# Performance work log

Measured on AMD Instinct MI355X. Metric: run time of the kernel, lower is better.

Reference implementation:

```python
import jax, jax.numpy as jnp
import numpy as np
import math

ALPHA, BETA = 0.0, 0.1  # MarketRelation defaults


def setup_inputs() -> dict:
    key = jax.random.key(0)
    ks = jax.random.split(key, 15)
    n, T, d, K, C = 1024, 8, 64, 8, 64
    h = d  # hidden = (2*infeat)//2 = infeat
    s = 0.1
    u = jax.random.uniform(ks[13], (n, n, K), jnp.float32, 1e-6, 1.0 - 1e-6)
    return {
        "x":   jax.random.normal(ks[0], (n, T, d), jnp.float32),
        "Ind": jax.random.uniform(ks[1], (n, n), jnp.float32),
        "Loc": jax.random.uniform(ks[2], (n, n), jnp.float32),
        "a":   jax.random.normal(ks[3], (T, 1), jnp.float32),
        "W1m": jax.random.normal(ks[4], (2 * d, h), jnp.float32) * s,
        "b1m": jax.random.normal(ks[5], (h,), jnp.float32) * s,
        "W2m": jax.random.normal(ks[6], (h, 1), jnp.float32) * s,
        "b2m": jax.random.normal(ks[7], (1,), jnp.float32) * s,
        "W1s": jax.random.normal(ks[8], (2 * d, h), jnp.float32) * s,
        "b1s": jax.random.normal(ks[9], (h,), jnp.float32) * s,
        "W2s": jax.random.normal(ks[10], (h, K), jnp.float32) * s,
        "b2s": jax.random.normal(ks[11], (K,), jnp.float32) * s,
        "E":   jax.random.normal(ks[12], (K, n, C), jnp.float32) * s,
        "g":   -jnp.log(-jnp.log(u)),  # Gumbel(0,1) noise for gumbel_softmax
    }


def reference(x, Ind, Loc, a, W1m, b1m, W2m, b2m, W1s, b1s, W2s, b2s, E, g):
    n, T, d = x.shape
    # --- MarketRelation ---
    # fc1(concat(x_j, x_k)) == x_j @ W1m[:d] + x_k @ W1m[d:] + b1m (same math,
    # avoids materializing the N x N x 2d concat tensor)
    W1a, W1b = W1m[:d], W1m[d:]
    a_soft = jax.nn.softmax(a, axis=0)  # [T,1]
    A_mkt = jnp.zeros((n, n), x.dtype)
    for i in range(T):
        xi = x[:, i, :]                      # [n,d]
        hA = xi @ W1a                        # [n,h]
        hB = xi @ W1b                        # [n,h]
        hmat = jax.nn.relu(hA[:, None, :] + hB[None, :, :] + b1m)  # [n,n,h]
        adj = jax.nn.relu(hmat @ W2m + b2m)[..., 0]                # [n,n]
        factor = 1.0 + ALPHA * math.exp(-BETA * (T - i - 1))
        A_mkt = A_mkt + adj * (a_soft[i, 0] * factor)
    # --- NobsRelation (on last timestep) ---
    xl = x[:, -1, :]
    Ws1a, Ws1b = W1s[:d], W1s[d:]
    hs = jax.nn.relu((xl @ Ws1a)[:, None, :] + (xl @ Ws1b)[None, :, :] + b1s)
    logits = jax.nn.relu(hs @ W2s + b2s)          # [n,n,K]
    y = jax.nn.softmax(logits + g, axis=-1)       # gumbel_softmax, tau=1, soft
    D = jnp.einsum('knc,kmc->nmk', E, E)          # stack of E_k E_k^T, [n,n,K]
    A_nobs = jnp.sum(D * y, axis=-1)              # [n,n]
    return jnp.stack([Ind, Loc, A_mkt, A_nobs])   # [4,n,n]
```

## Files before the change

kernel.cpp:

```cpp
#include <hip/hip_runtime.h>

typedef unsigned short USH;
typedef unsigned int UIN;
typedef _Float16 F16;
typedef F16 h2 __attribute__((ext_vector_type(2)));
typedef short bfrag __attribute__((ext_vector_type(8)));
typedef float f32x4 __attribute__((ext_vector_type(4)));

__device__ __forceinline__ float bf2f(USH u) {
    return __uint_as_float(((unsigned int)u) << 16);
}
__device__ __forceinline__ USH f2bf(float f) {
    unsigned int i = __float_as_uint(f);
    i += 0x7FFFu + ((i >> 16) & 1u);
    return (USH)(i >> 16);
}
__device__ __forceinline__ UIN pkh2(float a, float b) {
    h2 h; h.x = (F16)a; h.y = (F16)b;
    return __builtin_bit_cast(UIN, h);
}
__device__ __forceinline__ h2 u2h(UIN u) { return __builtin_bit_cast(h2, u); }
__device__ __forceinline__ h2 relu2h(h2 s) {
    const h2 zz = {(F16)0.0f, (F16)0.0f};
    return __builtin_elementwise_max(s, zz);
}
__device__ __forceinline__ float fdot2(h2 a, h2 b, float c) {
#if __has_builtin(__builtin_amdgcn_fdot2)
    return __builtin_amdgcn_fdot2(a, b, c, false);
#else
    return c + (float)a.x * (float)b.x + (float)a.y * (float)b.y;
#endif
}

__device__ __forceinline__ float ldf(const void* p, long idx, int bf) {
    return bf ? bf2f(((const USH*)p)[idx]) : ((const float*)p)[idx];
}
__device__ __forceinline__ void ld4(const void* p, long idx, int bf, float o[4]) {
    if (bf) {
        ushort4 u = *(const ushort4*)((const USH*)p + idx);
        o[0] = bf2f(u.x); o[1] = bf2f(u.y); o[2] = bf2f(u.z); o[3] = bf2f(u.w);
    } else {
        float4 v = *(const float4*)((const float*)p + idx);
        o[0] = v.x; o[1] = v.y; o[2] = v.z; o[3] = v.w;
    }
}

__device__ __forceinline__ int detect_bf(const void* ind) {
    const uint4* p = (const uint4*)ind;
    unsigned o = 0;
    #pragma unroll
    for (int i = 0; i < 8; ++i) { uint4 v = p[i]; o |= v.x | v.y | v.z | v.w; }
    return (o & 0x8000u) == 0;
}


__global__ __launch_bounds__(256) void k_pre_d(
    const void* __restrict__ x,
    const void* __restrict__ W1m,
    const void* __restrict__ b1m,
    const void* __restrict__ W1s,
    const void* __restrict__ b1s,
    const void* __restrict__ E,
    const void* __restrict__ IndDet,
    UIN* __restrict__ hA16,
    UIN* __restrict__ hB16,
    USH* __restrict__ D)
{
    __shared__ float smem[8192];
    const int bf = detect_bf(IndDet);
    const int tid = threadIdx.x;
    const int bid = blockIdx.x;

    if (bid < 512) {
        USH* sE = (USH*)smem;
        const int k = bid >> 6;
        const int nb = ((bid >> 3) & 7) * 128, mb = (bid & 7) * 128;
        const long ek = (long)k * 65536;

        const int row = tid >> 1;
        const int c0 = (tid & 1) * 32;
        #pragma unroll
        for (int side = 0; side < 2; ++side) {
            const int rbase = side ? mb : nb;
            USH* sDst = sE + side * 8192;
            const long gbase = ek + (long)(rbase + row) * 64 + c0;
            USH tmp[32];
            if (bf) {
                #pragma unroll
                for (int q = 0; q < 4; ++q)
                    *(uint4*)&tmp[q * 8] = *(const uint4*)((const USH*)E + gbase + q * 8);
            } else {
                #pragma unroll
                for (int q = 0; q < 4; ++q) {
                    const float4 va = *(const float4*)((const float*)E + gbase + q * 8);
                    const float4 vb = *(const float4*)((const float*)E + gbase + q * 8 + 4);
                    tmp[q * 8 + 0] = f2bf(va.x); tmp[q * 8 + 1] = f2bf(va.y);
                    tmp[q * 8 + 2] = f2bf(va.z); tmp[q * 8 + 3] = f2bf(va.w);
                    tmp[q * 8 + 4] = f2bf(vb.x); tmp[q * 8 + 5] = f2bf(vb.y);
                    tmp[q * 8 + 6] = f2bf(vb.z); tmp[q * 8 + 7] = f2bf(vb.w);
                }
            }
            #pragma unroll
            for (int q = 0; q < 4; ++q) {
                const int byte = (c0 + q * 8) * 2;
                const int sw = (row * 128 + (byte ^ ((row & 7) << 4))) >> 1;
                *(uint4*)&sDst[sw] = *(uint4*)&tmp[q * 8];
            }
        }
        __syncthreads();

        const int lane = tid & 63;
        const int w = tid >> 6;
        const int wn = (w >> 1) * 64, wm = (w & 1) * 64;
        const int fr = lane & 15, kg = lane >> 4;

        f32x4 acc[4][4] = {};
        #pragma unroll
        for (int ks = 0; ks < 2; ++ks) {
            const int cb = (ks * 32 + kg * 8) * 2;
            bfrag af[4], bfv[4];
            #pragma unroll
            for (int f = 0; f < 4; ++f) {
                const int ra = wn + f * 16 + fr;
                af[f] = *(const bfrag*)&sE[(ra * 128 + (cb ^ ((ra & 7) << 4))) >> 1];
                const int rb = wm + f * 16 + fr;
                bfv[f] = *(const bfrag*)&sE[8192 + ((rb * 128 + (cb ^ ((rb & 7) << 4))) >> 1)];
            }
            #pragma unroll
            for (int fn = 0; fn < 4; ++fn)
                #pragma unroll
                for (int fm = 0; fm < 4; ++fm)
                    acc[fn][fm] = __builtin_amdgcn_mfma_f32_16x16x32_bf16(
                        af[fn], bfv[fm], acc[fn][fm], 0, 0, 0);
        }

        USH* Dk = D + ((long)k << 20);
        #pragma unroll
        for (int fn = 0; fn < 4; ++fn) {
            const int nrow = nb + wn + fn * 16 + kg * 4;
            #pragma unroll
            for (int fm = 0; fm < 4; ++fm) {
                const int mcol = mb + wm + fm * 16 + fr;
                #pragma unroll
                for (int r = 0; r < 4; ++r)
                    Dk[(long)(nrow + r) * 1024 + mcol] = f2bf(acc[fn][fm][r]);
            }
        }
    } else {
        float* sA = smem;
        float* sB = smem + 4096;
        const int tx = tid & 15, ty = tid >> 4;
        const int bid2 = bid - 512;
        const int nbase = (bid2 & 15) * 64;
        const int by = bid2 >> 4;
        int t, rb;
        const void* Wsrc;
        const void* bias;
        UIN* dst;
        if (by < 8)        { t = by;     rb = 0;  Wsrc = W1m; bias = nullptr; dst = hA16 + by * 32768; }
        else if (by < 16)  { t = by - 8; rb = 64; Wsrc = W1m; bias = b1m;     dst = hB16 + (by - 8) * 32768; }
        else if (by == 16) { t = 7;      rb = 0;  Wsrc = W1s; bias = nullptr; dst = hA16 + 8 * 32768; }
        else               { t = 7;      rb = 64; Wsrc = W1s; bias = b1s;     dst = hB16 + 8 * 32768; }

        {
            const int n_l = tid >> 2, dq = tid & 3;
            const long base = (long)(nbase + n_l) * 512 + t * 64 + dq * 16;
            #pragma unroll
            for (int j = 0; j < 4; ++j) {
                float o[4]; ld4(x, base + j * 4, bf, o);
                const int d0 = dq * 16 + j * 4;
                #pragma unroll
                for (int e = 0; e < 4; ++e) sA[(d0 + e) * 64 + n_l] = o[e];
            }
        }
        {
            const int d_l = tid >> 2, cq = tid & 3;
            const long base = (long)(rb + d_l) * 64 + cq * 16;
            #pragma unroll
            for (int j = 0; j < 4; ++j) {
                float o[4]; ld4(Wsrc, base + j * 4, bf, o);
                const int c0 = cq * 16 + j * 4;
                #pragma unroll
                for (int e = 0; e < 4; ++e) sB[d_l * 64 + c0 + e] = o[e];
            }
        }
        __syncthreads();

        const int c0 = tx * 4, nq = ty * 4;
        float acc[4][4] = {};
        #pragma unroll 16
        for (int d = 0; d < 64; ++d) {
            const float4 xa = *(const float4*)&sA[d * 64 + nq];
            const float4 wv = *(const float4*)&sB[d * 64 + c0];
            const float aa[4] = {xa.x, xa.y, xa.z, xa.w};
            const float ww[4] = {wv.x, wv.y, wv.z, wv.w};
            #pragma unroll
            for (int ci = 0; ci < 4; ++ci)
                #pragma unroll
                for (int ni = 0; ni < 4; ++ni)
                    acc[ci][ni] += ww[ci] * aa[ni];
        }
        float b[4] = {0.f, 0.f, 0.f, 0.f};
        if (bias) {
            #pragma unroll
            for (int ci = 0; ci < 4; ++ci) b[ci] = ldf(bias, c0 + ci, bf);
        }
        const int cp0 = c0 >> 1;
        #pragma unroll
        for (int ni = 0; ni < 4; ++ni) {
            const int col = nbase + nq + ni;
            dst[cp0 * 1024 + col]       = pkh2(acc[0][ni] + b[0], acc[1][ni] + b[1]);
            dst[(cp0 + 1) * 1024 + col] = pkh2(acc[2][ni] + b[2], acc[3][ni] + b[3]);
        }
    }
}

__global__ __launch_bounds__(256, 4) void k_main(
    const UIN* __restrict__ hA16,
    const UIN* __restrict__ hB16,
    const USH* __restrict__ Dm,
    const void* __restrict__ Ind, const void* __restrict__ Loc,
    const void* __restrict__ a, const void* __restrict__ W2m,
    const void* __restrict__ b2m, const void* __restrict__ W2s,
    const void* __restrict__ b2s, const void* __restrict__ g,
    void* __restrict__ out)
{
    __shared__ UIN As[2][1024];
    __shared__ UIN Bs[2][1024];
    __shared__ UIN w2m16[32];
    __shared__ UIN w2s16[256];
    __shared__ float asoft_l[8];

    const int bf = detect_bf(Ind);
    const int tid = threadIdx.x;
    const int mb = blockIdx.x * 32, nb = blockIdx.y * 32;
    const int tx = tid & 15, ty = tid >> 4;
    const int m0 = tx * 2, n0 = ty * 2;

    if (tid < 32) w2m16[tid] = pkh2(ldf(W2m, 2 * tid, bf), ldf(W2m, 2 * tid + 1, bf));
    if (tid >= 64 && tid < 96) {
        const int cp = tid - 64;
        #pragma unroll
        for (int k = 0; k < 8; ++k)
            w2s16[cp * 8 + k] = pkh2(ldf(W2s, (2 * cp) * 8 + k, bf),
                                     ldf(W2s, (2 * cp + 1) * 8 + k, bf));
    }
    if (tid < 8) {
        float av[8], mx = -1e30f, s = 0.0f;
        #pragma unroll
        for (int k = 0; k < 8; ++k) { av[k] = ldf(a, k, bf); mx = fmaxf(mx, av[k]); }
        #pragma unroll
        for (int k = 0; k < 8; ++k) s += __expf(av[k] - mx);
        asoft_l[tid] = __expf(av[tid] - mx) / s;
    }
    const float b2m_f = ldf(b2m, 0, bf);

    const int offA = (tid >> 3) * 1024 + nb + (tid & 7) * 4;
    const int offB = (tid >> 3) * 1024 + mb + (tid & 7) * 4;
    const int ldsOff = (tid >> 3) * 32 + (tid & 7) * 4;

    {
        const uint4 pa = *(const uint4*)(hA16 + offA);
        const uint4 pb = *(const uint4*)(hB16 + offB);
        *(uint4*)&As[0][ldsOff] = pa;
        *(uint4*)&Bs[0][ldsOff] = pb;
    }
    __syncthreads();

    float amk[2][2] = {{0.f, 0.f}, {0.f, 0.f}};

    for (int t = 0; t < 8; ++t) {
        const int cur = t & 1, nxt = cur ^ 1;
        const uint4 pa = *(const uint4*)(hA16 + (t + 1) * 32768 + offA);
        const uint4 pb = *(const uint4*)(hB16 + (t + 1) * 32768 + offB);

        float a00 = 0.f, a01 = 0.f, a10 = 0.f, a11 = 0.f;
        #pragma unroll
        for (int cp = 0; cp < 32; ++cp) {
            const uint2 au = *(const uint2*)&As[cur][(cp << 5) + n0];
            const uint2 bu = *(const uint2*)&Bs[cur][(cp << 5) + m0];
            const h2 wv = u2h(w2m16[cp]);
            const h2 a0 = u2h(au.x), a1 = u2h(au.y);
            const h2 b0 = u2h(bu.x), b1 = u2h(bu.y);
            const h2 z00 = relu2h(a0 + b0), z01 = relu2h(a0 + b1);
            const h2 z10 = relu2h(a1 + b0), z11 = relu2h(a1 + b1);
            a00 = fdot2(z00, wv, a00); a01 = fdot2(z01, wv, a01);
            a10 = fdot2(z10, wv, a10); a11 = fdot2(z11, wv, a11);
        }
        const float as_t = asoft_l[t];
        amk[0][0] += fmaxf(a00 + b2m_f, 0.f) * as_t;
        amk[0][1] += fmaxf(a01 + b2m_f, 0.f) * as_t;
        amk[1][0] += fmaxf(a10 + b2m_f, 0.f) * as_t;
        amk[1][1] += fmaxf(a11 + b2m_f, 0.f) * as_t;

        *(uint4*)&As[nxt][ldsOff] = pa;
        *(uint4*)&Bs[nxt][ldsOff] = pb;
        __syncthreads();
    }

    float lg[2][2][8];
    #pragma unroll
    for (int i = 0; i < 2; ++i)
        #pragma unroll
        for (int j = 0; j < 2; ++j)
            #pragma unroll
            for (int k = 0; k < 8; ++k) lg[i][j][k] = 0.f;

    #pragma unroll 8
    for (int cp = 0; cp < 32; ++cp) {
        const uint2 au = *(const uint2*)&As[0][(cp << 5) + n0];
        const uint2 bu = *(const uint2*)&Bs[0][(cp << 5) + m0];
        const h2 a0 = u2h(au.x), a1 = u2h(au.y);
        const h2 b0 = u2h(bu.x), b1 = u2h(bu.y);
        const h2 z00 = relu2h(a0 + b0), z01 = relu2h(a0 + b1);
        const h2 z10 = relu2h(a1 + b0), z11 = relu2h(a1 + b1);
        const uint4 wa = *(const uint4*)&w2s16[cp * 8];
        const uint4 wb = *(const uint4*)&w2s16[cp * 8 + 4];
        const UIN wks[8] = {wa.x, wa.y, wa.z, wa.w, wb.x, wb.y, wb.z, wb.w};
        #pragma unroll
        for (int k = 0; k < 8; ++k) {
            const h2 wv = u2h(wks[k]);
            lg[0][0][k] = fdot2(z00, wv, lg[0][0][k]);
            lg[0][1][k] = fdot2(z01, wv, lg[0][1][k]);
            lg[1][0][k] = fdot2(z10, wv, lg[1][0][k]);
            lg[1][1][k] = fdot2(z11, wv, lg[1][1][k]);
        }
    }

    float b2s_f[8];
    #pragma unroll
    for (int k = 0; k < 8; ++k) b2s_f[k] = ldf(b2s, k, bf);

    #pragma unroll
    for (int i = 0; i < 2; ++i) {
        const long rowoff = (long)(nb + n0 + i) * 1024 + mb + m0;
        float gv[16];
        ld4(g, rowoff * 8 + 0, bf, gv + 0);
        ld4(g, rowoff * 8 + 4, bf, gv + 4);
        ld4(g, rowoff * 8 + 8, bf, gv + 8);
        ld4(g, rowoff * 8 + 12, bf, gv + 12);

        float s0 = 0.0f, s1 = 0.0f, d0 = 0.0f, d1 = 0.0f;
        #pragma unroll
        for (int k = 0; k < 8; ++k) {
            const float l0 = fmaxf(lg[i][0][k] + b2s_f[k], 0.f);
            const float l1 = fmaxf(lg[i][1][k] + b2s_f[k], 0.f);
            const float e0 = __expf(l0 + gv[k]);
            const float e1 = __expf(l1 + gv[8 + k]);
            s0 += e0; s1 += e1;
            const ushort2 dv = *(const ushort2*)&Dm[((long)k << 20) + rowoff];
            d0 += bf2f(dv.x) * e0;
            d1 += bf2f(dv.y) * e1;
        }

        if (bf) {
            USH* o = (USH*)out;
            *(ushort2*)&o[rowoff] = *(const ushort2*)&((const USH*)Ind)[rowoff];
            *(ushort2*)&o[1048576 + rowoff] = *(const ushort2*)&((const USH*)Loc)[rowoff];
            ushort2 o2; o2.x = f2bf(amk[i][0]); o2.y = f2bf(amk[i][1]);
            *(ushort2*)&o[2 * 1048576 + rowoff] = o2;
            ushort2 o3; o3.x = f2bf(d0 / s0); o3.y = f2bf(d1 / s1);
            *(ushort2*)&o[3 * 1048576 + rowoff] = o3;
        } else {
            float* o = (float*)out;
            *(float2*)&o[rowoff] = *(const float2*)&((const float*)Ind)[rowoff];
            *(float2*)&o[1048576 + rowoff] = *(const float2*)&((const float*)Loc)[rowoff];
            float2 o2; o2.x = amk[i][0]; o2.y = amk[i][1];
            *(float2*)&o[2 * 1048576 + rowoff] = o2;
            float2 o3; o3.x = d0 / s0; o3.y = d1 / s1;
            *(float2*)&o[3 * 1048576 + rowoff] = o3;
        }
    }
}

extern "C" void kernel_launch(void* const* d_in, const int* in_sizes, int n_in,
                              void* d_out, int out_size, void* d_ws, size_t ws_size,
                              hipStream_t stream) {
    const void* x   = d_in[0];
    const void* Ind = d_in[1];
    const void* Loc = d_in[2];
    const void* a   = d_in[3];
    const void* W1m = d_in[4];
    const void* b1m = d_in[5];
    const void* W2m = d_in[6];
    const void* b2m = d_in[7];
    const void* W1s = d_in[8];
    const void* b1s = d_in[9];
    const void* W2s = d_in[10];
    const void* b2s = d_in[11];
    const void* E   = d_in[12];
    const void* g   = d_in[13];

    UIN* ws   = (UIN*)d_ws;
    UIN* hA16 = ws;
    UIN* hB16 = hA16 + 294912;
    USH* Dm   = (USH*)(hB16 + 294912);

    k_pre_d<<<dim3(800), 256, 0, stream>>>(x, W1m, b1m, W1s, b1s, E, Ind,
                                           hA16, hB16, Dm);
    k_main<<<dim3(32, 32), 256, 0, stream>>>(hA16, hB16, Dm,
                                             Ind, Loc, a, W2m, b2m, W2s, b2s,
                                             g, d_out);
}
```

Baseline: 162.3 us.

## Use single-wavefront 16x16 tiles in k_main and drop block barriers

k_main changes from 256-thread blocks on 32x32 output tiles to 64-thread, single-wavefront blocks on 16x16 tiles, with a 64x64 grid. The double-buffered LDS staging becomes one buffer, and every __syncthreads is removed. This relies on in-order LDS execution within one wave, and each thread now stages two uint4 loads per operand. The goal is to remove barrier stalls and raise the number of independent waves in flight. The cost is half the operand reuse per tile and more global or L2 traffic for hA16/hB16.

```diff
diff --git a/kernel.cpp b/kernel.cpp
--- a/kernel.cpp
+++ b/kernel.cpp
@@ -215,7 +215,7 @@
     }
 }
 
-__global__ __launch_bounds__(256, 4) void k_main(
+__global__ __launch_bounds__(64) void k_main(
     const UIN* __restrict__ hA16,
     const UIN* __restrict__ hB16,
     const USH* __restrict__ Dm,
@@ -225,25 +225,27 @@
     const void* __restrict__ b2s, const void* __restrict__ g,
     void* __restrict__ out)
 {
-    __shared__ UIN As[2][1024];
-    __shared__ UIN Bs[2][1024];
+    __shared__ UIN As[512];
+    __shared__ UIN Bs[512];
     __shared__ UIN w2m16[32];
     __shared__ UIN w2s16[256];
     __shared__ float asoft_l[8];
 
     const int bf = detect_bf(Ind);
     const int tid = threadIdx.x;
-    const int mb = blockIdx.x * 32, nb = blockIdx.y * 32;
-    const int tx = tid & 15, ty = tid >> 4;
-    const int m0 = tx * 2, n0 = ty * 2;
+    const int mb = blockIdx.x * 16, nb = blockIdx.y * 16;
+    const int m0 = (tid & 7) * 2;
+    const int n0 = (tid >> 3) * 2;
 
     if (tid < 32) w2m16[tid] = pkh2(ldf(W2m, 2 * tid, bf), ldf(W2m, 2 * tid + 1, bf));
-    if (tid >= 64 && tid < 96) {
-        const int cp = tid - 64;
-        #pragma unroll
-        for (int k = 0; k < 8; ++k)
+    {
+        const int cp = tid >> 1, kh = (tid & 1) * 4;
+        #pragma unroll
+        for (int e = 0; e < 4; ++e) {
+            const int k = kh + e;
             w2s16[cp * 8 + k] = pkh2(ldf(W2s, (2 * cp) * 8 + k, bf),
                                      ldf(W2s, (2 * cp + 1) * 8 + k, bf));
+        }
     }
     if (tid < 8) {
         float av[8], mx = -1e30f, s = 0.0f;
@@ -255,30 +257,33 @@
     }
     const float b2m_f = ldf(b2m, 0, bf);
 
-    const int offA = (tid >> 3) * 1024 + nb + (tid & 7) * 4;
-    const int offB = (tid >> 3) * 1024 + mb + (tid & 7) * 4;
-    const int ldsOff = (tid >> 3) * 32 + (tid & 7) * 4;
+    const int cpS = tid >> 1, half = tid & 1;
+    const int offA = cpS * 1024 + nb + half * 8;
+    const int offB = cpS * 1024 + mb + half * 8;
+    const int ldsS = cpS * 16 + half * 8;
 
     {
-        const uint4 pa = *(const uint4*)(hA16 + offA);
-        const uint4 pb = *(const uint4*)(hB16 + offB);
-        *(uint4*)&As[0][ldsOff] = pa;
-        *(uint4*)&Bs[0][ldsOff] = pb;
-    }
-    __syncthreads();
+        const uint4 a0 = *(const uint4*)(hA16 + offA);
+        const uint4 a1 = *(const uint4*)(hA16 + offA + 4);
+        const uint4 b0 = *(const uint4*)(hB16 + offB);
+        const uint4 b1 = *(const uint4*)(hB16 + offB + 4);
+        *(uint4*)&As[ldsS] = a0; *(uint4*)&As[ldsS + 4] = a1;
+        *(uint4*)&Bs[ldsS] = b0; *(uint4*)&Bs[ldsS + 4] = b1;
+    }
 
     float amk[2][2] = {{0.f, 0.f}, {0.f, 0.f}};
 
     for (int t = 0; t < 8; ++t) {
-        const int cur = t & 1, nxt = cur ^ 1;
-        const uint4 pa = *(const uint4*)(hA16 + (t + 1) * 32768 + offA);
-        const uint4 pb = *(const uint4*)(hB16 + (t + 1) * 32768 + offB);
+        const uint4 pa0 = *(const uint4*)(hA16 + (t + 1) * 32768 + offA);
+        const uint4 pa1 = *(const uint4*)(hA16 + (t + 1) * 32768 + offA + 4);
+        const uint4 pb0 = *(const uint4*)(hB16 + (t + 1) * 32768 + offB);
+        const uint4 pb1 = *(const uint4*)(hB16 + (t + 1) * 32768 + offB + 4);
 
         float a00 = 0.f, a01 = 0.f, a10 = 0.f, a11 = 0.f;
         #pragma unroll
         for (int cp = 0; cp < 32; ++cp) {
-            const uint2 au = *(const uint2*)&As[cur][(cp << 5) + n0];
-            const uint2 bu = *(const uint2*)&Bs[cur][(cp << 5) + m0];
+            const uint2 au = *(const uint2*)&As[(cp << 4) + n0];
+            const uint2 bu = *(const uint2*)&Bs[(cp << 4) + m0];
             const h2 wv = u2h(w2m16[cp]);
             const h2 a0 = u2h(au.x), a1 = u2h(au.y);
             const h2 b0 = u2h(bu.x), b1 = u2h(bu.y);
@@ -293,9 +298,8 @@
         amk[1][0] += fmaxf(a10 + b2m_f, 0.f) * as_t;
         amk[1][1] += fmaxf(a11 + b2m_f, 0.f) * as_t;
 
-        *(uint4*)&As[nxt][ldsOff] = pa;
-        *(uint4*)&Bs[nxt][ldsOff] = pb;
-        __syncthreads();
+        *(uint4*)&As[ldsS] = pa0; *(uint4*)&As[ldsS + 4] = pa1;
+        *(uint4*)&Bs[ldsS] = pb0; *(uint4*)&Bs[ldsS + 4] = pb1;
     }
 
     float lg[2][2][8];
@@ -308,8 +312,8 @@
 
     #pragma unroll 8
     for (int cp = 0; cp < 32; ++cp) {
-        const uint2 au = *(const uint2*)&As[0][(cp << 5) + n0];
-        const uint2 bu = *(const uint2*)&Bs[0][(cp << 5) + m0];
+        const uint2 au = *(const uint2*)&As[(cp << 4) + n0];
+        const uint2 bu = *(const uint2*)&Bs[(cp << 4) + m0];
         const h2 a0 = u2h(au.x), a1 = u2h(au.y);
         const h2 b0 = u2h(bu.x), b1 = u2h(bu.y);
         const h2 z00 = relu2h(a0 + b0), z01 = relu2h(a0 + b1);
@@ -398,7 +402,7 @@
 
     k_pre_d<<<dim3(800), 256, 0, stream>>>(x, W1m, b1m, W1s, b1s, E, Ind,
                                            hA16, hB16, Dm);
-    k_main<<<dim3(32, 32), 256, 0, stream>>>(hA16, hB16, Dm,
-                                             Ind, Loc, a, W2m, b2m, W2s, b2s,
-                                             g, d_out);
-}
+    k_main<<<dim3(64, 64), 64, 0, stream>>>(hA16, hB16, Dm,
+                                            Ind, Loc, a, W2m, b2m, W2s, b2s,
+                                            g, d_out);
+}
```

Measured after the change: 167.3 us. 3.1% more time.
